# Kernel optimization log

Hardware: AMD Instinct MI355X
Metric: run time of the kernel (lower is better)

## Reference

```python
import jax, jax.numpy as jnp
import numpy as np

EMBED_DIM = 512
NUM_HEADS = 8
HEAD_DIM = EMBED_DIM // NUM_HEADS


def setup_inputs() -> dict:
    key = jax.random.key(0)
    k1, k2, kw, kb, kow, kob = jax.random.split(key, 6)
    B, L, C = 2, 2048, EMBED_DIM
    s = 1.0 / np.sqrt(C)
    return {
        "x1": jax.random.normal(k1, (B, L, C), dtype=jnp.float32),
        "x2": jax.random.normal(k2, (B, L, C), dtype=jnp.float32),
        # nn.Linear(embed_dim, 3*embed_dim): weight [3C, C], bias [3C]
        "qkv_w": jax.random.uniform(kw, (3 * C, C), jnp.float32, -s, s),
        "qkv_b": jax.random.uniform(kb, (3 * C,), jnp.float32, -s, s),
        # nn.Linear(embed_dim, embed_dim): weight [C, C], bias [C]
        "out_w": jax.random.uniform(kow, (C, C), jnp.float32, -s, s),
        "out_b": jax.random.uniform(kob, (C,), jnp.float32, -s, s),
    }


def _qkv(x, qkv_w, qkv_b):
    B, L, C = x.shape
    H, D = NUM_HEADS, C // NUM_HEADS
    # Linear: x @ W^T + b, then view(B, L, H, 3, D) and split along the '3' axis
    qkv = (jnp.einsum("blc,fc->blf", x, qkv_w) + qkv_b).reshape(B, L, H, 3, D)
    qkv = jnp.transpose(qkv, (3, 0, 2, 1, 4))  # [3, B, H, L, D]
    return qkv[0], qkv[1], qkv[2]


def _attend(q, k, v):
    # q,k,v: [B, H, L, D]; scale by 1/sqrt(D)
    scale = 1.0 / np.sqrt(q.shape[-1]).astype(np.float32)
    scores = jnp.einsum("bhqd,bhkd->bhqk", q, k) * scale  # [B,H,L,L]
    attn = jax.nn.softmax(scores, axis=-1)
    out = jnp.einsum("bhqk,bhkd->bhqd", attn, v)
    B, H, L, D = out.shape
    return jnp.transpose(out, (0, 2, 1, 3)).reshape(B, L, H * D)


def reference(x1, x2, qkv_w, qkv_b, out_w, out_b):
    q1, k1, v1 = _qkv(x1, qkv_w, qkv_b)
    q2, k2, v2 = _qkv(x2, qkv_w, qkv_b)
    out1 = _attend(q1, k2, v2)  # q from x1, k/v from x2
    out2 = _attend(q2, k1, v1)  # q from x2, k/v from x1
    out1 = jnp.einsum("blc,fc->blf", out1, out_w) + out_b
    out2 = jnp.einsum("blc,fc->blf", out2, out_w) + out_b
    return (out1, out2)
```

## Files before the change

kernel.cpp:

```cpp
#include <hip/hip_runtime.h>
#include <stdint.h>

typedef unsigned short u16;
typedef unsigned int u32;
typedef short bf16x8 __attribute__((ext_vector_type(8)));
typedef float f32x4 __attribute__((ext_vector_type(4)));

#define K_DIM 512

__device__ __forceinline__ u16 f2bf(float f) {
  union { float f; u32 u; } v; v.f = f;
  return (u16)((v.u + 0x8000u) >> 16);
}
__device__ __forceinline__ u32 pk2(float lo, float hi) {
  union { float f; u32 u; } a, b; a.f = lo; b.f = hi;
  return __builtin_amdgcn_perm(b.u + 0x8000u, a.u + 0x8000u, 0x07060302u);
}

__global__ void cvt_kernel(const float* __restrict__ x1, const float* __restrict__ x2,
                           const float* __restrict__ qkvw, const float* __restrict__ outw,
                           u16* __restrict__ xb, u16* __restrict__ wqkv, u16* __restrict__ wout) {
  int tid = blockIdx.x * 256 + threadIdx.x;
  const float4* src; u16* dst; int idx = tid;
  if (idx < 524288)        { src = (const float4*)x1;   dst = xb; }
  else if (idx < 1048576)  { src = (const float4*)x2;   dst = xb + 2097152; idx -= 524288; }
  else if (idx < 1245184)  { src = (const float4*)qkvw; dst = wqkv;         idx -= 1048576; }
  else                     { src = (const float4*)outw; dst = wout;         idx -= 1245184; }
  float4 v = src[idx];
  u32 d0 = pk2(v.x, v.y), d1 = pk2(v.z, v.w);
  *(uint2*)&dst[idx * 4] = make_uint2(d0, d1);
}

#define LDA 40

__global__ __launch_bounds__(256, 2) void qkv_gemm(
    const u16* __restrict__ A, const u16* __restrict__ W, const float* __restrict__ bias,
    u16* __restrict__ qb, u16* __restrict__ kb, u16* __restrict__ vtb) {
  __shared__ __align__(16) u16 As[128 * LDA];
  __shared__ __align__(16) u16 Bs[128 * LDA];
  const int t = threadIdx.x;
  const int m0 = blockIdx.x * 128, n0 = blockIdx.y * 128;
  const int lane = t & 63, l16 = lane & 15, quad = lane >> 4;
  const int w = t >> 6;
  const int wm = (w >> 1) * 64, wn = (w & 1) * 64;
  const int sr = t >> 2;
  const int sc = (t & 3) * 8;

  const u16* Ap = A + (m0 + sr) * K_DIM + sc;
  const u16* Wp = W + (n0 + sr) * K_DIM + sc;

  f32x4 acc[4][4];
#pragma unroll
  for (int i = 0; i < 4; ++i)
#pragma unroll
    for (int j = 0; j < 4; ++j) acc[i][j] = (f32x4){0.f, 0.f, 0.f, 0.f};

  uint4 ra0 = *(const uint4*)(Ap);
  uint4 ra1 = *(const uint4*)(Ap + 64 * K_DIM);
  uint4 rb0 = *(const uint4*)(Wp);
  uint4 rb1 = *(const uint4*)(Wp + 64 * K_DIM);

  for (int kt = 0; kt < 16; ++kt) {
    *(uint4*)&As[sr * LDA + sc] = ra0;
    *(uint4*)&As[(sr + 64) * LDA + sc] = ra1;
    *(uint4*)&Bs[sr * LDA + sc] = rb0;
    *(uint4*)&Bs[(sr + 64) * LDA + sc] = rb1;
    __syncthreads();
    if (kt < 15) {
      int ko = (kt + 1) * 32;
      ra0 = *(const uint4*)(Ap + ko);
      ra1 = *(const uint4*)(Ap + 64 * K_DIM + ko);
      rb0 = *(const uint4*)(Wp + ko);
      rb1 = *(const uint4*)(Wp + 64 * K_DIM + ko);
    }
    bf16x8 af[4], bfr[4];
#pragma unroll
    for (int mi = 0; mi < 4; ++mi)
      af[mi] = *(const bf16x8*)&As[(wm + mi * 16 + l16) * LDA + quad * 8];
#pragma unroll
    for (int ni = 0; ni < 4; ++ni)
      bfr[ni] = *(const bf16x8*)&Bs[(wn + ni * 16 + l16) * LDA + quad * 8];
#pragma unroll
    for (int mi = 0; mi < 4; ++mi)
#pragma unroll
      for (int ni = 0; ni < 4; ++ni)
        acc[mi][ni] = __builtin_amdgcn_mfma_f32_16x16x32_bf16(bfr[ni], af[mi], acc[mi][ni], 0, 0, 0);
    __syncthreads();
  }

  const int fbase = n0 + wn;
  const int h = fbase / 192;
  const int s = (fbase - h * 192) >> 6;
  float4 bv[4];
#pragma unroll
  for (int ni = 0; ni < 4; ++ni)
    bv[ni] = *(const float4*)&bias[fbase + ni * 16 + quad * 4];
  const int bh = m0 >> 11;
  const int lbase = (m0 & 2047) + wm;

  if (s == 2) {
    u16* dst = vtb + (size_t)((bh * 8 + h) * 64) * 2048;
#pragma unroll
    for (int mi = 0; mi < 4; ++mi) {
      int l = lbase + mi * 16 + l16;
#pragma unroll
      for (int ni = 0; ni < 4; ++ni)
#pragma unroll
        for (int r = 0; r < 4; ++r)
          dst[(ni * 16 + quad * 4 + r) * 2048 + l] = f2bf(acc[mi][ni][r] + bv[ni][r]);
    }
  } else {
    u16* dst = (s == 0 ? qb : kb) + (size_t)((bh * 8 + h) * 2048) * 64;
    const float sc2 = (s == 0) ? 0.18033688011112042f : 1.0f;
#pragma unroll
    for (int mi = 0; mi < 4; ++mi) {
      int l = lbase + mi * 16 + l16;
#pragma unroll
      for (int ni = 0; ni < 4; ++ni) {
        float v0 = (acc[mi][ni][0] + bv[ni][0]) * sc2;
        float v1 = (acc[mi][ni][1] + bv[ni][1]) * sc2;
        float v2 = (acc[mi][ni][2] + bv[ni][2]) * sc2;
        float v3 = (acc[mi][ni][3] + bv[ni][3]) * sc2;
        *(uint2*)&dst[(size_t)l * 64 + ni * 16 + quad * 4] = make_uint2(pk2(v0, v1), pk2(v2, v3));
      }
    }
  }
}

#define LQ 72
#define LP 80

__global__ __launch_bounds__(256, 2) void attn_kernel(
    const u16* __restrict__ qb, const u16* __restrict__ kb, const u16* __restrict__ vtb,
    u16* __restrict__ attnb) {
  __shared__ __align__(16) u16 Ks[64 * LQ];
  __shared__ __align__(16) u16 VTs[64 * LQ];
  __shared__ __align__(16) u16 Ps[128 * LP];

  const int t = threadIdx.x;
  const int w = t >> 6, lane = t & 63, l16 = lane & 15, quad = lane >> 4;
  const int bid = blockIdx.x;
  const int qt = bid & 15;
  const int comb = bid >> 4;
  const int h = comb & 7, bb = (comb >> 3) & 1, pair = comb >> 4;
  const int in_q = pair, in_kv = pair ^ 1;

  const u16* Qg = qb + (size_t)((in_q * 2 + bb) * 8 + h) * 2048 * 64;
  const u16* Kg = kb + (size_t)((in_kv * 2 + bb) * 8 + h) * 2048 * 64;
  const u16* Vg = vtb + (size_t)((in_kv * 2 + bb) * 8 + h) * 64 * 2048;

#pragma unroll
  for (int u = 0; u < 4; ++u) {
    int idx = u * 256 + t;
    int row = idx >> 3, seg = (idx & 7) * 8;
    *(uint4*)&Ps[row * LP + seg] = *(const uint4*)(Qg + (qt * 128 + row) * 64 + seg);
  }
  __syncthreads();
  bf16x8 qf[2][2];
#pragma unroll
  for (int mi = 0; mi < 2; ++mi)
#pragma unroll
    for (int ks = 0; ks < 2; ++ks)
      qf[mi][ks] = *(const bf16x8*)&Ps[(w * 32 + mi * 16 + l16) * LP + ks * 32 + quad * 8];

  f32x4 oacc[2][4];
  float rs[2] = {0.f, 0.f};
#pragma unroll
  for (int mi = 0; mi < 2; ++mi)
#pragma unroll
    for (int ni = 0; ni < 4; ++ni) oacc[mi][ni] = (f32x4){0.f, 0.f, 0.f, 0.f};

  u16* Pw = &Ps[w * 32 * LP];

  const int srow = t >> 3, sseg = (t & 7) * 8;
  uint4 rk0 = *(const uint4*)(Kg + srow * 64 + sseg);
  uint4 rk1 = *(const uint4*)(Kg + (srow + 32) * 64 + sseg);
  uint4 rv0 = *(const uint4*)(Vg + srow * 2048 + sseg);
  uint4 rv1 = *(const uint4*)(Vg + (srow + 32) * 2048 + sseg);

  for (int kt = 0; kt < 32; ++kt) {
    __syncthreads();
    *(uint4*)&Ks[srow * LQ + sseg] = rk0;
    *(uint4*)&Ks[(srow + 32) * LQ + sseg] = rk1;
    *(uint4*)&VTs[srow * LQ + sseg] = rv0;
    *(uint4*)&VTs[(srow + 32) * LQ + sseg] = rv1;
    __syncthreads();
    if (kt < 31) {
      int ko = (kt + 1) * 64;
      rk0 = *(const uint4*)(Kg + (ko + srow) * 64 + sseg);
      rk1 = *(const uint4*)(Kg + (ko + srow + 32) * 64 + sseg);
      rv0 = *(const uint4*)(Vg + srow * 2048 + ko + sseg);
      rv1 = *(const uint4*)(Vg + (srow + 32) * 2048 + ko + sseg);
    }

    f32x4 sacc[2][4];
#pragma unroll
    for (int mi = 0; mi < 2; ++mi)
#pragma unroll
      for (int ni = 0; ni < 4; ++ni) sacc[mi][ni] = (f32x4){0.f, 0.f, 0.f, 0.f};
#pragma unroll
    for (int ks = 0; ks < 2; ++ks) {
      bf16x8 kfr[4];
#pragma unroll
      for (int ni = 0; ni < 4; ++ni)
        kfr[ni] = *(const bf16x8*)&Ks[(ni * 16 + l16) * LQ + ks * 32 + quad * 8];
#pragma unroll
      for (int mi = 0; mi < 2; ++mi)
#pragma unroll
        for (int ni = 0; ni < 4; ++ni)
          sacc[mi][ni] = __builtin_amdgcn_mfma_f32_16x16x32_bf16(kfr[ni], qf[mi][ks], sacc[mi][ni], 0, 0, 0);
    }

#pragma unroll
    for (int mi = 0; mi < 2; ++mi)
#pragma unroll
      for (int ni = 0; ni < 4; ++ni) {
        float p0 = exp2f(sacc[mi][ni][0]);
        float p1 = exp2f(sacc[mi][ni][1]);
        float p2 = exp2f(sacc[mi][ni][2]);
        float p3 = exp2f(sacc[mi][ni][3]);
        rs[mi] += (p0 + p1) + (p2 + p3);
        *(uint2*)&Pw[(mi * 16 + l16) * LP + ni * 16 + quad * 4] = make_uint2(pk2(p0, p1), pk2(p2, p3));
      }

#pragma unroll
    for (int ks = 0; ks < 2; ++ks) {
      bf16x8 vf[4], pf[2];
#pragma unroll
      for (int ni = 0; ni < 4; ++ni)
        vf[ni] = *(const bf16x8*)&VTs[(ni * 16 + l16) * LQ + ks * 32 + quad * 8];
#pragma unroll
      for (int mi = 0; mi < 2; ++mi)
        pf[mi] = *(const bf16x8*)&Pw[(mi * 16 + l16) * LP + ks * 32 + quad * 8];
#pragma unroll
      for (int mi = 0; mi < 2; ++mi)
#pragma unroll
        for (int ni = 0; ni < 4; ++ni)
          oacc[mi][ni] = __builtin_amdgcn_mfma_f32_16x16x32_bf16(vf[ni], pf[mi], oacc[mi][ni], 0, 0, 0);
    }
  }

  float inv[2];
#pragma unroll
  for (int mi = 0; mi < 2; ++mi) {
    float s = rs[mi];
    s += __shfl_xor(s, 16);
    s += __shfl_xor(s, 32);
    inv[mi] = 1.0f / s;
  }
  const int mbase = in_q * 4096 + bb * 2048 + qt * 128 + w * 32;
#pragma unroll
  for (int mi = 0; mi < 2; ++mi) {
    int row = mbase + mi * 16 + l16;
#pragma unroll
    for (int ni = 0; ni < 4; ++ni) {
      float v0 = oacc[mi][ni][0] * inv[mi];
      float v1 = oacc[mi][ni][1] * inv[mi];
      float v2 = oacc[mi][ni][2] * inv[mi];
      float v3 = oacc[mi][ni][3] * inv[mi];
      *(uint2*)&attnb[(size_t)row * 512 + h * 64 + ni * 16 + quad * 4] =
          make_uint2(pk2(v0, v1), pk2(v2, v3));
    }
  }
}

__global__ __launch_bounds__(256, 2) void out_gemm(
    const u16* __restrict__ A, const u16* __restrict__ W, const float* __restrict__ bias,
    float* __restrict__ out) {
  __shared__ __align__(16) u16 As[64 * LDA];
  __shared__ __align__(16) u16 Bs[128 * LDA];
  const int t = threadIdx.x;
  const int m0 = blockIdx.x * 64, n0 = blockIdx.y * 128;
  const int lane = t & 63, l16 = lane & 15, quad = lane >> 4;
  const int w = t >> 6;
  const int wm = (w & 1) * 32, wn = (w >> 1) * 64;
  const int sr = t >> 2;
  const int sc = (t & 3) * 8;

  const u16* Ap = A + (m0 + sr) * K_DIM + sc;
  const u16* Wp = W + (n0 + sr) * K_DIM + sc;

  f32x4 acc[2][4];
#pragma unroll
  for (int i = 0; i < 2; ++i)
#pragma unroll
    for (int j = 0; j < 4; ++j) acc[i][j] = (f32x4){0.f, 0.f, 0.f, 0.f};

  uint4 ra0 = *(const uint4*)(Ap);
  uint4 rb0 = *(const uint4*)(Wp);
  uint4 rb1 = *(const uint4*)(Wp + 64 * K_DIM);

  for (int kt = 0; kt < 16; ++kt) {
    *(uint4*)&As[sr * LDA + sc] = ra0;
    *(uint4*)&Bs[sr * LDA + sc] = rb0;
    *(uint4*)&Bs[(sr + 64) * LDA + sc] = rb1;
    __syncthreads();
    if (kt < 15) {
      int ko = (kt + 1) * 32;
      ra0 = *(const uint4*)(Ap + ko);
      rb0 = *(const uint4*)(Wp + ko);
      rb1 = *(const uint4*)(Wp + 64 * K_DIM + ko);
    }
    bf16x8 af[2], bfr[4];
#pragma unroll
    for (int mi = 0; mi < 2; ++mi)
      af[mi] = *(const bf16x8*)&As[(wm + mi * 16 + l16) * LDA + quad * 8];
#pragma unroll
    for (int ni = 0; ni < 4; ++ni)
      bfr[ni] = *(const bf16x8*)&Bs[(wn + ni * 16 + l16) * LDA + quad * 8];
#pragma unroll
    for (int mi = 0; mi < 2; ++mi)
#pragma unroll
      for (int ni = 0; ni < 4; ++ni)
        acc[mi][ni] = __builtin_amdgcn_mfma_f32_16x16x32_bf16(af[mi], bfr[ni], acc[mi][ni], 0, 0, 0);
    __syncthreads();
  }

#pragma unroll
  for (int ni = 0; ni < 4; ++ni) {
    int f = n0 + wn + ni * 16 + l16;
    float bv = bias[f];
#pragma unroll
    for (int mi = 0; mi < 2; ++mi)
#pragma unroll
      for (int r = 0; r < 4; ++r) {
        int m = m0 + wm + mi * 16 + quad * 4 + r;
        out[(size_t)m * 512 + f] = acc[mi][ni][r] + bv;
      }
  }
}

extern "C" void kernel_launch(void* const* d_in, const int* in_sizes, int n_in,
                              void* d_out, int out_size, void* d_ws, size_t ws_size,
                              hipStream_t stream) {
  const float* x1   = (const float*)d_in[0];
  const float* x2   = (const float*)d_in[1];
  const float* qkvw = (const float*)d_in[2];
  const float* qkvb = (const float*)d_in[3];
  const float* outw = (const float*)d_in[4];
  const float* outb = (const float*)d_in[5];
  float* out = (float*)d_out;
  char* ws = (char*)d_ws;

  u16* xb    = (u16*)(ws + 0);
  u16* wqkv  = (u16*)(ws + 8388608);
  u16* wout  = (u16*)(ws + 9961472);
  u16* qb    = (u16*)(ws + 10485760);
  u16* kb    = (u16*)(ws + 18874368);
  u16* vtb   = (u16*)(ws + 27262976);
  u16* attnb = (u16*)(ws + 0);

  cvt_kernel<<<5120, 256, 0, stream>>>(x1, x2, qkvw, outw, xb, wqkv, wout);

  dim3 g1(64, 12);
  qkv_gemm<<<g1, 256, 0, stream>>>(xb, wqkv, qkvb, qb, kb, vtb);

  attn_kernel<<<512, 256, 0, stream>>>(qb, kb, vtb, attnb);

  dim3 g3(128, 4);
  out_gemm<<<g3, 256, 0, stream>>>(attnb, wout, outb, out);
}
```

Baseline: 178.0 us.

## Fuse fp32-to-bf16 conversion into GEMM tile loads and drop convert kernel

Removes the separate conversion kernel. The QKV and output GEMMs now load fp32 activations and weights directly from global memory and pack them to bf16 while staging into shared memory. This saves one launch and a full write and re-read of the bf16 copies, but the GEMMs read twice as many bytes per tile and weights are re-converted by every block. Launch-bound occupancy hints are also raised for all three compute kernels, which may constrain register allocation.

```diff
diff --git a/kernel.cpp b/kernel.cpp
--- a/kernel.cpp
+++ b/kernel.cpp
@@ -16,25 +16,15 @@
   union { float f; u32 u; } a, b; a.f = lo; b.f = hi;
   return __builtin_amdgcn_perm(b.u + 0x8000u, a.u + 0x8000u, 0x07060302u);
 }
-
-__global__ void cvt_kernel(const float* __restrict__ x1, const float* __restrict__ x2,
-                           const float* __restrict__ qkvw, const float* __restrict__ outw,
-                           u16* __restrict__ xb, u16* __restrict__ wqkv, u16* __restrict__ wout) {
-  int tid = blockIdx.x * 256 + threadIdx.x;
-  const float4* src; u16* dst; int idx = tid;
-  if (idx < 524288)        { src = (const float4*)x1;   dst = xb; }
-  else if (idx < 1048576)  { src = (const float4*)x2;   dst = xb + 2097152; idx -= 524288; }
-  else if (idx < 1245184)  { src = (const float4*)qkvw; dst = wqkv;         idx -= 1048576; }
-  else                     { src = (const float4*)outw; dst = wout;         idx -= 1245184; }
-  float4 v = src[idx];
-  u32 d0 = pk2(v.x, v.y), d1 = pk2(v.z, v.w);
-  *(uint2*)&dst[idx * 4] = make_uint2(d0, d1);
+__device__ __forceinline__ uint4 pk8(const float4& a, const float4& b) {
+  return make_uint4(pk2(a.x, a.y), pk2(a.z, a.w), pk2(b.x, b.y), pk2(b.z, b.w));
 }
 
 #define LDA 40
 
-__global__ __launch_bounds__(256, 2) void qkv_gemm(
-    const u16* __restrict__ A, const u16* __restrict__ W, const float* __restrict__ bias,
+__global__ __launch_bounds__(256, 3) void qkv_gemm(
+    const float* __restrict__ X1, const float* __restrict__ X2,
+    const float* __restrict__ W, const float* __restrict__ bias,
     u16* __restrict__ qb, u16* __restrict__ kb, u16* __restrict__ vtb) {
   __shared__ __align__(16) u16 As[128 * LDA];
   __shared__ __align__(16) u16 Bs[128 * LDA];
@@ -43,11 +33,13 @@
   const int lane = t & 63, l16 = lane & 15, quad = lane >> 4;
   const int w = t >> 6;
   const int wm = (w >> 1) * 64, wn = (w & 1) * 64;
-  const int sr = t >> 2;
-  const int sc = (t & 3) * 8;
-
-  const u16* Ap = A + (m0 + sr) * K_DIM + sc;
-  const u16* Wp = W + (n0 + sr) * K_DIM + sc;
+
+  const float* A = (m0 < 4096) ? X1 : X2;
+  const int mrow = m0 & 4095;
+
+  const int srow = t >> 1, sc0 = (t & 1) * 16;
+  const float* Apf = A + (size_t)(mrow + srow) * K_DIM + sc0;
+  const float* Wpf = W + (size_t)(n0 + srow) * K_DIM + sc0;
 
   f32x4 acc[4][4];
 #pragma unroll
@@ -55,23 +47,26 @@
 #pragma unroll
     for (int j = 0; j < 4; ++j) acc[i][j] = (f32x4){0.f, 0.f, 0.f, 0.f};
 
-  uint4 ra0 = *(const uint4*)(Ap);
-  uint4 ra1 = *(const uint4*)(Ap + 64 * K_DIM);
-  uint4 rb0 = *(const uint4*)(Wp);
-  uint4 rb1 = *(const uint4*)(Wp + 64 * K_DIM);
+  float4 a4[4], w4[4];
+#pragma unroll
+  for (int j = 0; j < 4; ++j) {
+    a4[j] = ((const float4*)Apf)[j];
+    w4[j] = ((const float4*)Wpf)[j];
+  }
 
   for (int kt = 0; kt < 16; ++kt) {
-    *(uint4*)&As[sr * LDA + sc] = ra0;
-    *(uint4*)&As[(sr + 64) * LDA + sc] = ra1;
-    *(uint4*)&Bs[sr * LDA + sc] = rb0;
-    *(uint4*)&Bs[(sr + 64) * LDA + sc] = rb1;
+    *(uint4*)&As[srow * LDA + sc0]     = pk8(a4[0], a4[1]);
+    *(uint4*)&As[srow * LDA + sc0 + 8] = pk8(a4[2], a4[3]);
+    *(uint4*)&Bs[srow * LDA + sc0]     = pk8(w4[0], w4[1]);
+    *(uint4*)&Bs[srow * LDA + sc0 + 8] = pk8(w4[2], w4[3]);
     __syncthreads();
     if (kt < 15) {
       int ko = (kt + 1) * 32;
-      ra0 = *(const uint4*)(Ap + ko);
-      ra1 = *(const uint4*)(Ap + 64 * K_DIM + ko);
-      rb0 = *(const uint4*)(Wp + ko);
-      rb1 = *(const uint4*)(Wp + 64 * K_DIM + ko);
+#pragma unroll
+      for (int j = 0; j < 4; ++j) {
+        a4[j] = ((const float4*)(Apf + ko))[j];
+        w4[j] = ((const float4*)(Wpf + ko))[j];
+      }
     }
     bf16x8 af[4], bfr[4];
 #pragma unroll
@@ -130,7 +125,7 @@
 #define LQ 72
 #define LP 80
 
-__global__ __launch_bounds__(256, 2) void attn_kernel(
+__global__ __launch_bounds__(256, 4) void attn_kernel(
     const u16* __restrict__ qb, const u16* __restrict__ kb, const u16* __restrict__ vtb,
     u16* __restrict__ attnb) {
   __shared__ __align__(16) u16 Ks[64 * LQ];
@@ -264,8 +259,8 @@
   }
 }
 
-__global__ __launch_bounds__(256, 2) void out_gemm(
-    const u16* __restrict__ A, const u16* __restrict__ W, const float* __restrict__ bias,
+__global__ __launch_bounds__(256, 4) void out_gemm(
+    const u16* __restrict__ A, const float* __restrict__ W, const float* __restrict__ bias,
     float* __restrict__ out) {
   __shared__ __align__(16) u16 As[64 * LDA];
   __shared__ __align__(16) u16 Bs[128 * LDA];
@@ -274,11 +269,11 @@
   const int lane = t & 63, l16 = lane & 15, quad = lane >> 4;
   const int w = t >> 6;
   const int wm = (w & 1) * 32, wn = (w >> 1) * 64;
-  const int sr = t >> 2;
-  const int sc = (t & 3) * 8;
-
-  const u16* Ap = A + (m0 + sr) * K_DIM + sc;
-  const u16* Wp = W + (n0 + sr) * K_DIM + sc;
+
+  const int ar = t >> 2, ac = (t & 3) * 8;
+  const u16* Ap = A + (size_t)(m0 + ar) * K_DIM + ac;
+  const int wr = t >> 1, wc0 = (t & 1) * 16;
+  const float* Wpf = W + (size_t)(n0 + wr) * K_DIM + wc0;
 
   f32x4 acc[2][4];
 #pragma unroll
@@ -286,20 +281,21 @@
 #pragma unroll
     for (int j = 0; j < 4; ++j) acc[i][j] = (f32x4){0.f, 0.f, 0.f, 0.f};
 
-  uint4 ra0 = *(const uint4*)(Ap);
-  uint4 rb0 = *(const uint4*)(Wp);
-  uint4 rb1 = *(const uint4*)(Wp + 64 * K_DIM);
+  uint4 ra = *(const uint4*)Ap;
+  float4 w4[4];
+#pragma unroll
+  for (int j = 0; j < 4; ++j) w4[j] = ((const float4*)Wpf)[j];
 
   for (int kt = 0; kt < 16; ++kt) {
-    *(uint4*)&As[sr * LDA + sc] = ra0;
-    *(uint4*)&Bs[sr * LDA + sc] = rb0;
-    *(uint4*)&Bs[(sr + 64) * LDA + sc] = rb1;
+    *(uint4*)&As[ar * LDA + ac] = ra;
+    *(uint4*)&Bs[wr * LDA + wc0]     = pk8(w4[0], w4[1]);
+    *(uint4*)&Bs[wr * LDA + wc0 + 8] = pk8(w4[2], w4[3]);
     __syncthreads();
     if (kt < 15) {
       int ko = (kt + 1) * 32;
-      ra0 = *(const uint4*)(Ap + ko);
-      rb0 = *(const uint4*)(Wp + ko);
-      rb1 = *(const uint4*)(Wp + 64 * K_DIM + ko);
+      ra = *(const uint4*)(Ap + ko);
+#pragma unroll
+      for (int j = 0; j < 4; ++j) w4[j] = ((const float4*)(Wpf + ko))[j];
     }
     bf16x8 af[2], bfr[4];
 #pragma unroll
@@ -342,21 +338,16 @@
   float* out = (float*)d_out;
   char* ws = (char*)d_ws;
 
-  u16* xb    = (u16*)(ws + 0);
-  u16* wqkv  = (u16*)(ws + 8388608);
-  u16* wout  = (u16*)(ws + 9961472);
-  u16* qb    = (u16*)(ws + 10485760);
-  u16* kb    = (u16*)(ws + 18874368);
-  u16* vtb   = (u16*)(ws + 27262976);
-  u16* attnb = (u16*)(ws + 0);
-
-  cvt_kernel<<<5120, 256, 0, stream>>>(x1, x2, qkvw, outw, xb, wqkv, wout);
+  u16* qb    = (u16*)(ws + 0);
+  u16* kb    = (u16*)(ws + 8388608);
+  u16* vtb   = (u16*)(ws + 16777216);
+  u16* attnb = (u16*)(ws + 25165824);
 
   dim3 g1(64, 12);
-  qkv_gemm<<<g1, 256, 0, stream>>>(xb, wqkv, qkvb, qb, kb, vtb);
+  qkv_gemm<<<g1, 256, 0, stream>>>(x1, x2, qkvw, qkvb, qb, kb, vtb);
 
   attn_kernel<<<512, 256, 0, stream>>>(qb, kb, vtb, attnb);
 
   dim3 g3(128, 4);
-  out_gemm<<<g3, 256, 0, stream>>>(attnb, wout, outb, out);
-}
+  out_gemm<<<g3, 256, 0, stream>>>(attnb, outw, outb, out);
+}
```

Result: slower. 193.9 us (+8.9%).

## Double-buffer shared-memory tiles in GEMM and attention kernels

Applied to the files above, without the earlier changes.

Converts the shared-memory K/V and GEMM A/B tiles into ping-pong buffers, so the next tile is written to the alternate buffer while the current one is consumed. This cuts the per-iteration barriers from two to one and lets global loads run two stages ahead. The QKV GEMM launch bound is also raised to 3 blocks per CU. In exchange, shared memory use doubles, which may limit occupancy, and register pressure rises under the tighter launch bound.

```diff
diff --git a/kernel.cpp b/kernel.cpp
--- a/kernel.cpp
+++ b/kernel.cpp
@@ -27,27 +27,25 @@
   else if (idx < 1245184)  { src = (const float4*)qkvw; dst = wqkv;         idx -= 1048576; }
   else                     { src = (const float4*)outw; dst = wout;         idx -= 1245184; }
   float4 v = src[idx];
-  u32 d0 = pk2(v.x, v.y), d1 = pk2(v.z, v.w);
-  *(uint2*)&dst[idx * 4] = make_uint2(d0, d1);
+  *(uint2*)&dst[idx * 4] = make_uint2(pk2(v.x, v.y), pk2(v.z, v.w));
 }
 
 #define LDA 40
 
-__global__ __launch_bounds__(256, 2) void qkv_gemm(
+__global__ __launch_bounds__(256, 3) void qkv_gemm(
     const u16* __restrict__ A, const u16* __restrict__ W, const float* __restrict__ bias,
     u16* __restrict__ qb, u16* __restrict__ kb, u16* __restrict__ vtb) {
-  __shared__ __align__(16) u16 As[128 * LDA];
-  __shared__ __align__(16) u16 Bs[128 * LDA];
+  __shared__ __align__(16) u16 As[2][128 * LDA];
+  __shared__ __align__(16) u16 Bs[2][128 * LDA];
   const int t = threadIdx.x;
   const int m0 = blockIdx.x * 128, n0 = blockIdx.y * 128;
   const int lane = t & 63, l16 = lane & 15, quad = lane >> 4;
   const int w = t >> 6;
   const int wm = (w >> 1) * 64, wn = (w & 1) * 64;
-  const int sr = t >> 2;
-  const int sc = (t & 3) * 8;
-
-  const u16* Ap = A + (m0 + sr) * K_DIM + sc;
-  const u16* Wp = W + (n0 + sr) * K_DIM + sc;
+  const int sr = t >> 2, sc = (t & 3) * 8;
+
+  const u16* Ap = A + (size_t)(m0 + sr) * K_DIM + sc;
+  const u16* Wp = W + (size_t)(n0 + sr) * K_DIM + sc;
 
   f32x4 acc[4][4];
 #pragma unroll
@@ -59,15 +57,26 @@
   uint4 ra1 = *(const uint4*)(Ap + 64 * K_DIM);
   uint4 rb0 = *(const uint4*)(Wp);
   uint4 rb1 = *(const uint4*)(Wp + 64 * K_DIM);
+  *(uint4*)&As[0][sr * LDA + sc] = ra0;
+  *(uint4*)&As[0][(sr + 64) * LDA + sc] = ra1;
+  *(uint4*)&Bs[0][sr * LDA + sc] = rb0;
+  *(uint4*)&Bs[0][(sr + 64) * LDA + sc] = rb1;
+  ra0 = *(const uint4*)(Ap + 32);
+  ra1 = *(const uint4*)(Ap + 64 * K_DIM + 32);
+  rb0 = *(const uint4*)(Wp + 32);
+  rb1 = *(const uint4*)(Wp + 64 * K_DIM + 32);
+  __syncthreads();
 
   for (int kt = 0; kt < 16; ++kt) {
-    *(uint4*)&As[sr * LDA + sc] = ra0;
-    *(uint4*)&As[(sr + 64) * LDA + sc] = ra1;
-    *(uint4*)&Bs[sr * LDA + sc] = rb0;
-    *(uint4*)&Bs[(sr + 64) * LDA + sc] = rb1;
-    __syncthreads();
+    const int cur = kt & 1, nxt = cur ^ 1;
     if (kt < 15) {
-      int ko = (kt + 1) * 32;
+      *(uint4*)&As[nxt][sr * LDA + sc] = ra0;
+      *(uint4*)&As[nxt][(sr + 64) * LDA + sc] = ra1;
+      *(uint4*)&Bs[nxt][sr * LDA + sc] = rb0;
+      *(uint4*)&Bs[nxt][(sr + 64) * LDA + sc] = rb1;
+    }
+    if (kt < 14) {
+      int ko = (kt + 2) * 32;
       ra0 = *(const uint4*)(Ap + ko);
       ra1 = *(const uint4*)(Ap + 64 * K_DIM + ko);
       rb0 = *(const uint4*)(Wp + ko);
@@ -76,10 +85,10 @@
     bf16x8 af[4], bfr[4];
 #pragma unroll
     for (int mi = 0; mi < 4; ++mi)
-      af[mi] = *(const bf16x8*)&As[(wm + mi * 16 + l16) * LDA + quad * 8];
+      af[mi] = *(const bf16x8*)&As[cur][(wm + mi * 16 + l16) * LDA + quad * 8];
 #pragma unroll
     for (int ni = 0; ni < 4; ++ni)
-      bfr[ni] = *(const bf16x8*)&Bs[(wn + ni * 16 + l16) * LDA + quad * 8];
+      bfr[ni] = *(const bf16x8*)&Bs[cur][(wn + ni * 16 + l16) * LDA + quad * 8];
 #pragma unroll
     for (int mi = 0; mi < 4; ++mi)
 #pragma unroll
@@ -133,8 +142,8 @@
 __global__ __launch_bounds__(256, 2) void attn_kernel(
     const u16* __restrict__ qb, const u16* __restrict__ kb, const u16* __restrict__ vtb,
     u16* __restrict__ attnb) {
-  __shared__ __align__(16) u16 Ks[64 * LQ];
-  __shared__ __align__(16) u16 VTs[64 * LQ];
+  __shared__ __align__(16) u16 Ks[2][64 * LQ];
+  __shared__ __align__(16) u16 VTs[2][64 * LQ];
   __shared__ __align__(16) u16 Ps[128 * LP];
 
   const int t = threadIdx.x;
@@ -155,38 +164,48 @@
     int row = idx >> 3, seg = (idx & 7) * 8;
     *(uint4*)&Ps[row * LP + seg] = *(const uint4*)(Qg + (qt * 128 + row) * 64 + seg);
   }
-  __syncthreads();
-  bf16x8 qf[2][2];
-#pragma unroll
-  for (int mi = 0; mi < 2; ++mi)
-#pragma unroll
-    for (int ks = 0; ks < 2; ++ks)
-      qf[mi][ks] = *(const bf16x8*)&Ps[(w * 32 + mi * 16 + l16) * LP + ks * 32 + quad * 8];
-
-  f32x4 oacc[2][4];
-  float rs[2] = {0.f, 0.f};
-#pragma unroll
-  for (int mi = 0; mi < 2; ++mi)
-#pragma unroll
-    for (int ni = 0; ni < 4; ++ni) oacc[mi][ni] = (f32x4){0.f, 0.f, 0.f, 0.f};
-
-  u16* Pw = &Ps[w * 32 * LP];
 
   const int srow = t >> 3, sseg = (t & 7) * 8;
   uint4 rk0 = *(const uint4*)(Kg + srow * 64 + sseg);
   uint4 rk1 = *(const uint4*)(Kg + (srow + 32) * 64 + sseg);
   uint4 rv0 = *(const uint4*)(Vg + srow * 2048 + sseg);
   uint4 rv1 = *(const uint4*)(Vg + (srow + 32) * 2048 + sseg);
+  *(uint4*)&Ks[0][srow * LQ + sseg] = rk0;
+  *(uint4*)&Ks[0][(srow + 32) * LQ + sseg] = rk1;
+  *(uint4*)&VTs[0][srow * LQ + sseg] = rv0;
+  *(uint4*)&VTs[0][(srow + 32) * LQ + sseg] = rv1;
+  rk0 = *(const uint4*)(Kg + (64 + srow) * 64 + sseg);
+  rk1 = *(const uint4*)(Kg + (64 + srow + 32) * 64 + sseg);
+  rv0 = *(const uint4*)(Vg + srow * 2048 + 64 + sseg);
+  rv1 = *(const uint4*)(Vg + (srow + 32) * 2048 + 64 + sseg);
+  __syncthreads();
+
+  bf16x8 qf[2][2];
+#pragma unroll
+  for (int mi = 0; mi < 2; ++mi)
+#pragma unroll
+    for (int ks = 0; ks < 2; ++ks)
+      qf[mi][ks] = *(const bf16x8*)&Ps[(w * 32 + mi * 16 + l16) * LP + ks * 32 + quad * 8];
+
+  f32x4 oacc[2][4];
+  float rs[2] = {0.f, 0.f};
+#pragma unroll
+  for (int mi = 0; mi < 2; ++mi)
+#pragma unroll
+    for (int ni = 0; ni < 4; ++ni) oacc[mi][ni] = (f32x4){0.f, 0.f, 0.f, 0.f};
+
+  u16* Pw = &Ps[w * 32 * LP];
 
   for (int kt = 0; kt < 32; ++kt) {
-    __syncthreads();
-    *(uint4*)&Ks[srow * LQ + sseg] = rk0;
-    *(uint4*)&Ks[(srow + 32) * LQ + sseg] = rk1;
-    *(uint4*)&VTs[srow * LQ + sseg] = rv0;
-    *(uint4*)&VTs[(srow + 32) * LQ + sseg] = rv1;
-    __syncthreads();
+    const int cur = kt & 1, nxt = cur ^ 1;
     if (kt < 31) {
-      int ko = (kt + 1) * 64;
+      *(uint4*)&Ks[nxt][srow * LQ + sseg] = rk0;
+      *(uint4*)&Ks[nxt][(srow + 32) * LQ + sseg] = rk1;
+      *(uint4*)&VTs[nxt][srow * LQ + sseg] = rv0;
+      *(uint4*)&VTs[nxt][(srow + 32) * LQ + sseg] = rv1;
+    }
+    if (kt < 30) {
+      int ko = (kt + 2) * 64;
       rk0 = *(const uint4*)(Kg + (ko + srow) * 64 + sseg);
       rk1 = *(const uint4*)(Kg + (ko + srow + 32) * 64 + sseg);
       rv0 = *(const uint4*)(Vg + srow * 2048 + ko + sseg);
@@ -203,7 +222,7 @@
       bf16x8 kfr[4];
 #pragma unroll
       for (int ni = 0; ni < 4; ++ni)
-        kfr[ni] = *(const bf16x8*)&Ks[(ni * 16 + l16) * LQ + ks * 32 + quad * 8];
+        kfr[ni] = *(const bf16x8*)&Ks[cur][(ni * 16 + l16) * LQ + ks * 32 + quad * 8];
 #pragma unroll
       for (int mi = 0; mi < 2; ++mi)
 #pragma unroll
@@ -228,7 +247,7 @@
       bf16x8 vf[4], pf[2];
 #pragma unroll
       for (int ni = 0; ni < 4; ++ni)
-        vf[ni] = *(const bf16x8*)&VTs[(ni * 16 + l16) * LQ + ks * 32 + quad * 8];
+        vf[ni] = *(const bf16x8*)&VTs[cur][(ni * 16 + l16) * LQ + ks * 32 + quad * 8];
 #pragma unroll
       for (int mi = 0; mi < 2; ++mi)
         pf[mi] = *(const bf16x8*)&Pw[(mi * 16 + l16) * LP + ks * 32 + quad * 8];
@@ -238,6 +257,7 @@
         for (int ni = 0; ni < 4; ++ni)
           oacc[mi][ni] = __builtin_amdgcn_mfma_f32_16x16x32_bf16(vf[ni], pf[mi], oacc[mi][ni], 0, 0, 0);
     }
+    __syncthreads();
   }
 
   float inv[2];
@@ -267,18 +287,18 @@
 __global__ __launch_bounds__(256, 2) void out_gemm(
     const u16* __restrict__ A, const u16* __restrict__ W, const float* __restrict__ bias,
     float* __restrict__ out) {
-  __shared__ __align__(16) u16 As[64 * LDA];
-  __shared__ __align__(16) u16 Bs[128 * LDA];
+  __shared__ __align__(16) u16 As[2][64 * LDA];
+  __shared__ __align__(16) u16 Bs[2][128 * LDA];
   const int t = threadIdx.x;
   const int m0 = blockIdx.x * 64, n0 = blockIdx.y * 128;
   const int lane = t & 63, l16 = lane & 15, quad = lane >> 4;
   const int w = t >> 6;
   const int wm = (w & 1) * 32, wn = (w >> 1) * 64;
-  const int sr = t >> 2;
-  const int sc = (t & 3) * 8;
-
-  const u16* Ap = A + (m0 + sr) * K_DIM + sc;
-  const u16* Wp = W + (n0 + sr) * K_DIM + sc;
+  const int ar = t >> 2, ac = (t & 3) * 8;
+  const int sr = t >> 2, sc = (t & 3) * 8;
+
+  const u16* Ap = A + (size_t)(m0 + ar) * K_DIM + ac;
+  const u16* Wp = W + (size_t)(n0 + sr) * K_DIM + sc;
 
   f32x4 acc[2][4];
 #pragma unroll
@@ -286,28 +306,37 @@
 #pragma unroll
     for (int j = 0; j < 4; ++j) acc[i][j] = (f32x4){0.f, 0.f, 0.f, 0.f};
 
-  uint4 ra0 = *(const uint4*)(Ap);
+  uint4 ra = *(const uint4*)Ap;
   uint4 rb0 = *(const uint4*)(Wp);
   uint4 rb1 = *(const uint4*)(Wp + 64 * K_DIM);
+  *(uint4*)&As[0][ar * LDA + ac] = ra;
+  *(uint4*)&Bs[0][sr * LDA + sc] = rb0;
+  *(uint4*)&Bs[0][(sr + 64) * LDA + sc] = rb1;
+  ra = *(const uint4*)(Ap + 32);
+  rb0 = *(const uint4*)(Wp + 32);
+  rb1 = *(const uint4*)(Wp + 64 * K_DIM + 32);
+  __syncthreads();
 
   for (int kt = 0; kt < 16; ++kt) {
-    *(uint4*)&As[sr * LDA + sc] = ra0;
-    *(uint4*)&Bs[sr * LDA + sc] = rb0;
-    *(uint4*)&Bs[(sr + 64) * LDA + sc] = rb1;
-    __syncthreads();
+    const int cur = kt & 1, nxt = cur ^ 1;
     if (kt < 15) {
-      int ko = (kt + 1) * 32;
-      ra0 = *(const uint4*)(Ap + ko);
+      *(uint4*)&As[nxt][ar * LDA + ac] = ra;
+      *(uint4*)&Bs[nxt][sr * LDA + sc] = rb0;
+      *(uint4*)&Bs[nxt][(sr + 64) * LDA + sc] = rb1;
+    }
+    if (kt < 14) {
+      int ko = (kt + 2) * 32;
+      ra = *(const uint4*)(Ap + ko);
       rb0 = *(const uint4*)(Wp + ko);
       rb1 = *(const uint4*)(Wp + 64 * K_DIM + ko);
     }
     bf16x8 af[2], bfr[4];
 #pragma unroll
     for (int mi = 0; mi < 2; ++mi)
-      af[mi] = *(const bf16x8*)&As[(wm + mi * 16 + l16) * LDA + quad * 8];
+      af[mi] = *(const bf16x8*)&As[cur][(wm + mi * 16 + l16) * LDA + quad * 8];
 #pragma unroll
     for (int ni = 0; ni < 4; ++ni)
-      bfr[ni] = *(const bf16x8*)&Bs[(wn + ni * 16 + l16) * LDA + quad * 8];
+      bfr[ni] = *(const bf16x8*)&Bs[cur][(wn + ni * 16 + l16) * LDA + quad * 8];
 #pragma unroll
     for (int mi = 0; mi < 2; ++mi)
 #pragma unroll
```

After: 175.5 us. No clear change (-1.4%).
